# Kernel optimization log

Measured on AMD Instinct MI355X. Metric: run time of the kernel, lower is better.

Reference implementation:

```python
import jax, jax.numpy as jnp
import numpy as np

B, T, C, H, NC = 512, 256, 512, 512, 96  # batch, encoder steps, channels, hidden, num classes


def setup_inputs() -> dict:
    key = jax.random.key(0)
    ks = jax.random.split(key, 12)
    def w(k, shape, fan):
        return (jax.random.normal(k, shape, jnp.float32) / np.sqrt(fan)).astype(jnp.float32)
    labels = jax.random.randint(ks[0], (B,), 0, NC)
    return {
        "prev_h": jax.random.normal(ks[1], (B, H), jnp.float32),
        "prev_c": jax.random.normal(ks[2], (B, H), jnp.float32),
        "batch_H": jax.random.normal(ks[3], (B, T, C), jnp.float32),
        "char_onehots": jax.nn.one_hot(labels, NC, dtype=jnp.float32),
        "Wi": w(ks[4], (C, H), C),            # i2h kernel (no bias)
        "Wh": w(ks[5], (H, H), H),            # h2h kernel
        "bh": jnp.zeros((H,), jnp.float32),    # h2h bias
        "Ws": w(ks[6], (H, 1), H),            # score kernel (no bias)
        "K": w(ks[7], (C + NC, 4 * H), C + NC),  # LSTM input kernel (i,f,g,o)
        "R": w(ks[8], (H, 4 * H), H),            # LSTM recurrent kernel
        "b": jnp.zeros((4 * H,), jnp.float32),    # LSTM bias
    }


def reference(prev_h, prev_c, batch_H, char_onehots, Wi, Wh, bh, Ws, K, R, b):
    # Additive (Bahdanau) attention
    proj = jnp.einsum('btc,ch->bth', batch_H, Wi)                  # [B,T,H]
    hp = prev_h @ Wh + bh                                          # [B,H]
    e = jnp.einsum('bth,h->bt', jnp.tanh(proj + hp[:, None, :]), Ws[:, 0])  # [B,T]
    alpha = jax.nn.softmax(e, axis=1)                              # [B,T]
    context = jnp.einsum('bt,btc->bc', alpha, batch_H)             # [B,C]
    # LSTMCell step (keras gate order: i, f, g, o; sigmoid recurrent act, tanh act)
    x = jnp.concatenate([context, char_onehots], axis=1)           # [B,C+NC]
    z = x @ K + prev_h @ R + b                                     # [B,4H]
    i, f, g, o = jnp.split(z, 4, axis=1)
    c_new = jax.nn.sigmoid(f) * prev_c + jax.nn.sigmoid(i) * jnp.tanh(g)
    h_new = jax.nn.sigmoid(o) * jnp.tanh(c_new)
    return (h_new, c_new, alpha[:, :, None])  # ((h,c), alpha[B,T,1])
```

## Files before the change

kernel.cpp:

```cpp
#include <hip/hip_runtime.h>
#include <hip/hip_bf16.h>
#include <stdint.h>

#define KFULL 1120
#define N4H   2048
#define MTOT  131072

typedef float f32x4 __attribute__((ext_vector_type(4)));
typedef __bf16 bf16x8 __attribute__((ext_vector_type(8)));
typedef unsigned short u16;

__device__ __forceinline__ u16 f2bf_bits(float f){
  __bf16 b = (__bf16)f;
  union { __bf16 b; u16 u; } cv; cv.b = b;
  return cv.u;
}
__device__ __forceinline__ float sigf(float x){ return 1.f / (1.f + __expf(-x)); }
__device__ __forceinline__ float tanh_fast(float x){ return 1.f - 2.f / (__expf(2.f * x) + 1.f); }
__device__ __forceinline__ int swz(int row){ return (row ^ (row >> 2)) & 3; }

__global__ void prep_w(const float* __restrict__ Wi, const float* __restrict__ Wh,
                       const float* __restrict__ Km, const float* __restrict__ R,
                       u16* __restrict__ wiT, u16* __restrict__ whT, u16* __restrict__ wfT){
  int idx = blockIdx.x * 256 + threadIdx.x;
  if (idx < 524288){
    const float* src = (idx < 262144) ? Wi : Wh;
    u16* dst = (idx < 262144) ? wiT : whT;
    int e = idx & 262143;
    int n = e & 511, kk = (e >> 9) & 31, s = e >> 14;
    float v = src[(size_t)(s * 32 + kk) * 512 + n];
    int dkk = (idx < 262144) ? kk
            : ((kk & 7) | ((((kk >> 3) ^ swz(n)) & 3) << 3));
    dst[((size_t)s * 512 + n) * 32 + dkk] = f2bf_bits(v);
  } else {
    int e = idx - 524288;
    if (e >= 35 * 2048 * 32) return;
    int n = e & 2047, kk = (e >> 11) & 31, s = e >> 16;
    int k = s * 32 + kk;
    float v = (k < 608) ? Km[(size_t)k * 2048 + n] : R[(size_t)(k - 608) * 2048 + n];
    int dkk = (kk & 7) | ((((kk >> 3) ^ swz(n)) & 3) << 3);
    wfT[((size_t)s * 2048 + n) * 32 + dkk] = f2bf_bits(v);
  }
}

__global__ void prep_x(const float* __restrict__ onehots, const float* __restrict__ prev_h,
                       float* __restrict__ x_full){
  int idx = blockIdx.x * 256 + threadIdx.x;
  if (idx >= 512 * 608) return;
  int b = idx / 608, c = idx % 608;
  float v = (c < 96) ? onehots[b * 96 + c] : prev_h[b * 512 + (c - 96)];
  x_full[(size_t)b * KFULL + 512 + c] = v;
}

__launch_bounds__(256, 3)
__global__ void gemm_small(const float* __restrict__ A, int lda, int ksteps,
                           const u16* __restrict__ Bt, int ntot,
                           float* __restrict__ outp, size_t partStride){
  __shared__ u16 smA[128 * 32];
  __shared__ u16 smB[128 * 32];

  const int tid  = threadIdx.x;
  const int lane = tid & 63, w = tid >> 6;
  const int wr = w >> 1, wc = w & 1;
  const int fr = lane & 15, g = lane >> 4;
  const int m0 = blockIdx.x * 128;
  const int n0 = blockIdx.y * 128;
  const int s0 = blockIdx.z * ksteps;
  outp += (size_t)blockIdx.z * partStride;

  f32x4 acc[4][4] = {};

  const int ar = tid >> 2;
  const int ac = (tid & 3) * 8;
  const float* ap = A + (size_t)(m0 + ar) * lda + ac;
  const int sz  = swz(ar);
  const int ab0 = ar * 64 + (((tid & 3) ^ sz) << 4);
  const int ab1 = ab0 + 64 * 64;

  for (int s = 0; s < ksteps; ++s){
    const int kc = (s0 + s) * 32;
    const char* bsrc = (const char*)Bt + ((size_t)(s0 + s) * ntot + n0) * 64;
    #pragma unroll
    for (int j = 0; j < 2; ++j){
      int off = w * 2048 + j * 1024;
      __builtin_amdgcn_global_load_lds(
        (const __attribute__((address_space(1))) void*)(bsrc + off + lane * 16),
        (__attribute__((address_space(3))) void*)((char*)smB + off),
        16, 0, 0);
    }
    float4 a0 = *(const float4*)(ap + kc);
    float4 a1 = *(const float4*)(ap + kc + 4);
    float4 a2 = *(const float4*)(ap + (size_t)64 * lda + kc);
    float4 a3 = *(const float4*)(ap + (size_t)64 * lda + kc + 4);
    bf16x8 w0, w1;
    w0[0]=(__bf16)a0.x; w0[1]=(__bf16)a0.y; w0[2]=(__bf16)a0.z; w0[3]=(__bf16)a0.w;
    w0[4]=(__bf16)a1.x; w0[5]=(__bf16)a1.y; w0[6]=(__bf16)a1.z; w0[7]=(__bf16)a1.w;
    w1[0]=(__bf16)a2.x; w1[1]=(__bf16)a2.y; w1[2]=(__bf16)a2.z; w1[3]=(__bf16)a2.w;
    w1[4]=(__bf16)a3.x; w1[5]=(__bf16)a3.y; w1[6]=(__bf16)a3.z; w1[7]=(__bf16)a3.w;
    *(bf16x8*)((char*)smA + ab0) = w0;
    *(bf16x8*)((char*)smA + ab1) = w1;
    __syncthreads();

    bf16x8 af[4];
    #pragma unroll
    for (int m = 0; m < 4; ++m){
      int rl = wr * 64 + m * 16 + fr;
      af[m] = *(const bf16x8*)((const char*)smA + rl * 64 + ((g ^ swz(rl)) << 4));
    }
    #pragma unroll
    for (int n = 0; n < 4; ++n){
      int nl = wc * 64 + n * 16 + fr;
      bf16x8 bfv = *(const bf16x8*)((const char*)smB + nl * 64 + ((g ^ swz(nl)) << 4));
      #pragma unroll
      for (int m = 0; m < 4; ++m)
        acc[m][n] = __builtin_amdgcn_mfma_f32_16x16x32_bf16(af[m], bfv, acc[m][n], 0, 0, 0);
    }
    __syncthreads();
  }

  #pragma unroll
  for (int n = 0; n < 4; ++n){
    int col = n0 + wc * 64 + n * 16 + fr;
    #pragma unroll
    for (int m = 0; m < 4; ++m){
      int row = m0 + wr * 64 + m * 16 + g * 4;
      #pragma unroll
      for (int j = 0; j < 4; ++j)
        outp[(size_t)(row + j) * ntot + col] = acc[m][n][j];
    }
  }
}

__launch_bounds__(256, 2)
__global__ void gemm_attn(const float* __restrict__ A,
                          const u16* __restrict__ Bt,
                          const float* __restrict__ hpart,
                          const float* __restrict__ bh,
                          const float* __restrict__ Wsv,
                          float* __restrict__ epart){
  __shared__ u16 smA[16][64 * 32];

  const int tid  = threadIdx.x;
  const int lane = tid & 63, w = tid >> 6;
  const int fr = lane & 15, g = lane >> 4;
  const int bid = blockIdx.x;
  const int m0 = (bid >> 1) * 64;
  const int nb = bid & 1;
  const int n0 = nb * 256;
  const int b  = m0 >> 8;

  const int arow = tid >> 2;
  const float* ag = A + (size_t)(m0 + arow) * 512 + (tid & 3) * 8;
  const int awbase = arow * 64 + (((tid & 3) ^ swz(arow)) << 4);
  float4 av[32];
  #pragma unroll
  for (int s = 0; s < 16; ++s){
    av[2 * s]     = *(const float4*)(ag + s * 32);
    av[2 * s + 1] = *(const float4*)(ag + s * 32 + 4);
  }
  #pragma unroll
  for (int s = 0; s < 16; ++s){
    bf16x8 v;
    v[0]=(__bf16)av[2*s].x;   v[1]=(__bf16)av[2*s].y;
    v[2]=(__bf16)av[2*s].z;   v[3]=(__bf16)av[2*s].w;
    v[4]=(__bf16)av[2*s+1].x; v[5]=(__bf16)av[2*s+1].y;
    v[6]=(__bf16)av[2*s+1].z; v[7]=(__bf16)av[2*s+1].w;
    *(bf16x8*)((char*)&smA[s][0] + awbase) = v;
  }

  float hpv[4], wsv[4];
  #pragma unroll
  for (int n = 0; n < 4; ++n){
    int col = n0 + w * 64 + n * 16 + fr;
    float h = bh[col];
    #pragma unroll
    for (int p = 0; p < 4; ++p) h += hpart[(size_t)p * 262144 + (size_t)b * 512 + col];
    hpv[n] = h;
    wsv[n] = Wsv[col];
  }

  __syncthreads();

  const u16* bbase = Bt + ((size_t)(n0 + w * 64 + fr)) * 32 + g * 8;
  bf16x8 bA[4], bB[4];
  #pragma unroll
  for (int nf = 0; nf < 4; ++nf)
    bA[nf] = *(const bf16x8*)(bbase + (size_t)nf * 16 * 32);

  f32x4 acc[4][4] = {};

  #pragma unroll
  for (int s = 0; s < 16; ++s){
    if (s + 1 < 16){
      if ((s & 1) == 0){
        #pragma unroll
        for (int nf = 0; nf < 4; ++nf)
          bB[nf] = *(const bf16x8*)(bbase + ((size_t)(s + 1) * 512 + nf * 16) * 32);
      } else {
        #pragma unroll
        for (int nf = 0; nf < 4; ++nf)
          bA[nf] = *(const bf16x8*)(bbase + ((size_t)(s + 1) * 512 + nf * 16) * 32);
      }
    }
    bf16x8 af[4];
    #pragma unroll
    for (int m = 0; m < 4; ++m){
      int rl = m * 16 + fr;
      af[m] = *(const bf16x8*)((const char*)&smA[s][0] + rl * 64 + ((g ^ swz(rl)) << 4));
    }
    #pragma unroll
    for (int n = 0; n < 4; ++n){
      bf16x8 bfv = ((s & 1) == 0) ? bA[n] : bB[n];
      #pragma unroll
      for (int m = 0; m < 4; ++m)
        acc[m][n] = __builtin_amdgcn_mfma_f32_16x16x32_bf16(af[m], bfv, acc[m][n], 0, 0, 0);
    }
  }

  float p[16] = {};
  #pragma unroll
  for (int n = 0; n < 4; ++n){
    #pragma unroll
    for (int m = 0; m < 4; ++m)
      #pragma unroll
      for (int j = 0; j < 4; ++j)
        p[m * 4 + j] += tanh_fast(acc[m][n][j] + hpv[n]) * wsv[n];
  }
  #pragma unroll
  for (int mask = 1; mask < 16; mask <<= 1)
    #pragma unroll
    for (int i = 0; i < 16; ++i)
      p[i] += __shfl_xor(p[i], mask);

  float* smRed = (float*)&smA[0][0];
  __syncthreads();
  if (fr == 0){
    #pragma unroll
    for (int m = 0; m < 4; ++m)
      #pragma unroll
      for (int j = 0; j < 4; ++j)
        smRed[w * 64 + m * 16 + g * 4 + j] = p[m * 4 + j];
  }
  __syncthreads();
  if (tid < 64)
    epart[(size_t)nb * MTOT + m0 + tid] =
      smRed[tid] + smRed[64 + tid] + smRed[128 + tid] + smRed[192 + tid];
}

__global__ void ctx_softmax(const float* __restrict__ epart, const float* __restrict__ batch_H,
                            float* __restrict__ x_full, float* __restrict__ alpha_out){
  __shared__ float sa[256];
  __shared__ float red[4], red2[4];
  __shared__ f32x4 sred[8][32];
  int b = blockIdx.x, q = blockIdx.y, tid = threadIdx.x;

  float e = epart[(size_t)b * 256 + tid] + epart[MTOT + (size_t)b * 256 + tid];
  float m = e;
  #pragma unroll
  for (int mask = 1; mask < 64; mask <<= 1) m = fmaxf(m, __shfl_xor(m, mask));
  int w = tid >> 6;
  if ((tid & 63) == 0) red[w] = m;
  __syncthreads();
  m = fmaxf(fmaxf(red[0], red[1]), fmaxf(red[2], red[3]));
  float ev = __expf(e - m);
  float s = ev;
  #pragma unroll
  for (int mask = 1; mask < 64; mask <<= 1) s += __shfl_xor(s, mask);
  if ((tid & 63) == 0) red2[w] = s;
  __syncthreads();
  s = red2[0] + red2[1] + red2[2] + red2[3];
  float a = ev / s;
  sa[tid] = a;
  if (q == 0) alpha_out[(size_t)b * 256 + tid] = a;
  __syncthreads();

  int c4 = tid & 31, tq = tid >> 5;
  const float4* bhp = (const float4*)(batch_H + (size_t)b * 131072) + (size_t)tq * 32 * 128 + q * 32 + c4;
  f32x4 acc = {0.f, 0.f, 0.f, 0.f};
  #pragma unroll 4
  for (int t = 0; t < 32; ++t){
    float av = sa[tq * 32 + t];
    float4 v = bhp[(size_t)t * 128];
    acc[0] += av * v.x; acc[1] += av * v.y; acc[2] += av * v.z; acc[3] += av * v.w;
  }
  sred[tq][c4] = acc;
  __syncthreads();
  if (tid < 32){
    f32x4 o = sred[0][tid];
    #pragma unroll
    for (int r = 1; r < 8; ++r){
      f32x4 v = sred[r][tid];
      o[0] += v[0]; o[1] += v[1]; o[2] += v[2]; o[3] += v[3];
    }
    float4 st; st.x = o[0]; st.y = o[1]; st.z = o[2]; st.w = o[3];
    *(float4*)(x_full + (size_t)b * KFULL + q * 128 + tid * 4) = st;
  }
}

__global__ void gates_k(const float* __restrict__ zpart, const float* __restrict__ bias,
                        const float* __restrict__ prev_c, float* __restrict__ out){
  int idx = blockIdx.x * 256 + threadIdx.x;
  int b = idx >> 9, h = idx & 511;
  float zi = bias[h], zf = bias[512 + h], zg = bias[1024 + h], zo = bias[1536 + h];
  #pragma unroll
  for (int p = 0; p < 5; ++p){
    const float* zr = zpart + (size_t)p * 1048576 + (size_t)b * N4H;
    zi += zr[h]; zf += zr[512 + h]; zg += zr[1024 + h]; zo += zr[1536 + h];
  }
  float c = sigf(zf) * prev_c[idx] + sigf(zi) * tanh_fast(zg);
  float hn = sigf(zo) * tanh_fast(c);
  out[idx] = hn;
  out[262144 + idx] = c;
}

extern "C" void kernel_launch(void* const* d_in, const int* in_sizes, int n_in,
                              void* d_out, int out_size, void* d_ws, size_t ws_size,
                              hipStream_t stream){
  const float* prev_h  = (const float*)d_in[0];
  const float* prev_c  = (const float*)d_in[1];
  const float* batch_H = (const float*)d_in[2];
  const float* onehots = (const float*)d_in[3];
  const float* Wi      = (const float*)d_in[4];
  const float* Wh      = (const float*)d_in[5];
  const float* bh      = (const float*)d_in[6];
  const float* Ws      = (const float*)d_in[7];
  const float* Km      = (const float*)d_in[8];
  const float* R       = (const float*)d_in[9];
  const float* bb      = (const float*)d_in[10];
  float* out = (float*)d_out;

  char* ws = (char*)d_ws;
  u16*  wiT    = (u16*)(ws + 0);
  u16*  whT    = (u16*)(ws + 524288);
  u16*  wfT    = (u16*)(ws + 1048576);
  float* hpart = (float*)(ws + 5636096);
  float* epart = (float*)(ws + 9830400);
  float* x_full= (float*)(ws + 11927552);
  float* zpart = (float*)(ws + 14221312);

  float* alpha = out + 524288;

  prep_w<<<11008, 256, 0, stream>>>(Wi, Wh, Km, R, wiT, whT, wfT);
  prep_x<<<1216, 256, 0, stream>>>(onehots, prev_h, x_full);
  gemm_small<<<dim3(4, 4, 4), 256, 0, stream>>>(prev_h, 512, 4, whT, 512,
                                                hpart, 262144);
  gemm_attn<<<4096, 256, 0, stream>>>(batch_H, wiT, hpart, bh, Ws, epart);
  ctx_softmax<<<dim3(512, 4), 256, 0, stream>>>(epart, batch_H, x_full, alpha);
  gemm_small<<<dim3(4, 16, 5), 256, 0, stream>>>(x_full, KFULL, 7, wfT, N4H,
                                                 zpart, 1048576);
  gates_k<<<1024, 256, 0, stream>>>(zpart, bb, prev_c, out);
}
```

Baseline: 245.4 us.

## Restructure attention GEMM with double-buffered LDS pipeline and larger tiles

The attention projection GEMM now uses 512-thread blocks with 128x256 tiles. B tiles are streamed into double-buffered LDS with global_load_lds, and A tiles are prefetched through registers in a software pipeline over K chunks of 64. The Wi weights are pre-laid out in a swizzled 64-wide K tiled format, and block IDs are remapped for locality. The aim is to hide global-load latency and raise reuse of A and B per block. The cost is more LDS per block and reliance on manual waitcnt ordering.

```diff
diff --git a/kernel.cpp b/kernel.cpp
--- a/kernel.cpp
+++ b/kernel.cpp
@@ -21,17 +21,20 @@
 
 __global__ void prep_w(const float* __restrict__ Wi, const float* __restrict__ Wh,
                        const float* __restrict__ Km, const float* __restrict__ R,
-                       u16* __restrict__ wiT, u16* __restrict__ whT, u16* __restrict__ wfT){
+                       u16* __restrict__ wiT2, u16* __restrict__ whT, u16* __restrict__ wfT){
   int idx = blockIdx.x * 256 + threadIdx.x;
-  if (idx < 524288){
-    const float* src = (idx < 262144) ? Wi : Wh;
-    u16* dst = (idx < 262144) ? wiT : whT;
-    int e = idx & 262143;
+  if (idx < 262144){
+    int col = idx & 511, kk = (idx >> 9) & 63, t = idx >> 15;
+    float v = Wi[(size_t)(t * 64 + kk) * 512 + col];
+    size_t dst = ((size_t)(t * 2 + (col >> 8)) * 256 + (col & 255)) * 64
+               + (size_t)(((kk >> 3) ^ (col & 7)) * 8 + (kk & 7));
+    wiT2[dst] = f2bf_bits(v);
+  } else if (idx < 524288){
+    int e = idx - 262144;
     int n = e & 511, kk = (e >> 9) & 31, s = e >> 14;
-    float v = src[(size_t)(s * 32 + kk) * 512 + n];
-    int dkk = (idx < 262144) ? kk
-            : ((kk & 7) | ((((kk >> 3) ^ swz(n)) & 3) << 3));
-    dst[((size_t)s * 512 + n) * 32 + dkk] = f2bf_bits(v);
+    float v = Wh[(size_t)(s * 32 + kk) * 512 + n];
+    int dkk = (kk & 7) | ((((kk >> 3) ^ swz(n)) & 3) << 3);
+    whT[((size_t)s * 512 + n) * 32 + dkk] = f2bf_bits(v);
   } else {
     int e = idx - 524288;
     if (e >= 35 * 2048 * 32) return;
@@ -131,47 +134,31 @@
   }
 }
 
-__launch_bounds__(256, 2)
+__launch_bounds__(512, 2)
 __global__ void gemm_attn(const float* __restrict__ A,
-                          const u16* __restrict__ Bt,
+                          const u16* __restrict__ Bt2,
                           const float* __restrict__ hpart,
                           const float* __restrict__ bh,
                           const float* __restrict__ Wsv,
                           float* __restrict__ epart){
-  __shared__ u16 smA[16][64 * 32];
+  __shared__ u16 bufA[2][128 * 64];
+  __shared__ u16 bufB[2][256 * 64];
+  __shared__ float smRed[4][128];
 
   const int tid  = threadIdx.x;
   const int lane = tid & 63, w = tid >> 6;
+  const int wr = w >> 2, wc = w & 3;
   const int fr = lane & 15, g = lane >> 4;
-  const int bid = blockIdx.x;
-  const int m0 = (bid >> 1) * 64;
-  const int nb = bid & 1;
-  const int n0 = nb * 256;
+
+  const int sid = (blockIdx.x & 7) * 256 + (blockIdx.x >> 3);
+  const int mb = sid >> 1, nb = sid & 1;
+  const int m0 = mb * 128, n0 = nb * 256;
   const int b  = m0 >> 8;
 
-  const int arow = tid >> 2;
-  const float* ag = A + (size_t)(m0 + arow) * 512 + (tid & 3) * 8;
-  const int awbase = arow * 64 + (((tid & 3) ^ swz(arow)) << 4);
-  float4 av[32];
-  #pragma unroll
-  for (int s = 0; s < 16; ++s){
-    av[2 * s]     = *(const float4*)(ag + s * 32);
-    av[2 * s + 1] = *(const float4*)(ag + s * 32 + 4);
-  }
-  #pragma unroll
-  for (int s = 0; s < 16; ++s){
-    bf16x8 v;
-    v[0]=(__bf16)av[2*s].x;   v[1]=(__bf16)av[2*s].y;
-    v[2]=(__bf16)av[2*s].z;   v[3]=(__bf16)av[2*s].w;
-    v[4]=(__bf16)av[2*s+1].x; v[5]=(__bf16)av[2*s+1].y;
-    v[6]=(__bf16)av[2*s+1].z; v[7]=(__bf16)av[2*s+1].w;
-    *(bf16x8*)((char*)&smA[s][0] + awbase) = v;
-  }
-
   float hpv[4], wsv[4];
   #pragma unroll
   for (int n = 0; n < 4; ++n){
-    int col = n0 + w * 64 + n * 16 + fr;
+    int col = n0 + wc * 64 + n * 16 + fr;
     float h = bh[col];
     #pragma unroll
     for (int p = 0; p < 4; ++p) h += hpart[(size_t)p * 262144 + (size_t)b * 512 + col];
@@ -179,43 +166,92 @@
     wsv[n] = Wsv[col];
   }
 
-  __syncthreads();
-
-  const u16* bbase = Bt + ((size_t)(n0 + w * 64 + fr)) * 32 + g * 8;
-  bf16x8 bA[4], bB[4];
-  #pragma unroll
-  for (int nf = 0; nf < 4; ++nf)
-    bA[nf] = *(const bf16x8*)(bbase + (size_t)nf * 16 * 32);
+  const int arow = tid >> 2, q = tid & 3;
+  const float* ag = A + (size_t)(m0 + arow) * 512 + q * 16;
+  const int aw0 = arow * 128 + (((2 * q)     ^ (arow & 7)) << 4);
+  const int aw1 = arow * 128 + (((2 * q + 1) ^ (arow & 7)) << 4);
+
+  const int fs = fr & 7;
 
   f32x4 acc[4][4] = {};
-
-  #pragma unroll
-  for (int s = 0; s < 16; ++s){
-    if (s + 1 < 16){
-      if ((s & 1) == 0){
-        #pragma unroll
-        for (int nf = 0; nf < 4; ++nf)
-          bB[nf] = *(const bf16x8*)(bbase + ((size_t)(s + 1) * 512 + nf * 16) * 32);
-      } else {
-        #pragma unroll
-        for (int nf = 0; nf < 4; ++nf)
-          bA[nf] = *(const bf16x8*)(bbase + ((size_t)(s + 1) * 512 + nf * 16) * 32);
-      }
-    }
-    bf16x8 af[4];
-    #pragma unroll
-    for (int m = 0; m < 4; ++m){
-      int rl = m * 16 + fr;
-      af[m] = *(const bf16x8*)((const char*)&smA[s][0] + rl * 64 + ((g ^ swz(rl)) << 4));
-    }
-    #pragma unroll
-    for (int n = 0; n < 4; ++n){
-      bf16x8 bfv = ((s & 1) == 0) ? bA[n] : bB[n];
-      #pragma unroll
-      for (int m = 0; m < 4; ++m)
-        acc[m][n] = __builtin_amdgcn_mfma_f32_16x16x32_bf16(af[m], bfv, acc[m][n], 0, 0, 0);
-    }
-  }
+  float4 paE[4], paO[4];
+
+#define ISSUE_B(t, c) do {                                                  \
+    const char* bsrc = (const char*)Bt2 + ((size_t)((t) * 2 + nb)) * 32768; \
+    _Pragma("unroll")                                                       \
+    for (int j = 0; j < 4; ++j){                                            \
+      int off = w * 4096 + j * 1024;                                        \
+      __builtin_amdgcn_global_load_lds(                                     \
+        (const __attribute__((address_space(1))) void*)(bsrc + off + lane * 16), \
+        (__attribute__((address_space(3))) void*)((char*)&bufB[c][0] + off),\
+        16, 0, 0);                                                          \
+    }                                                                       \
+  } while(0)
+
+#define ISSUE_A(t, R) do {                                                  \
+    const float* s_ = ag + (size_t)(t) * 64;                                \
+    R[0] = *(const float4*)(s_);                                            \
+    R[1] = *(const float4*)(s_ + 4);                                        \
+    R[2] = *(const float4*)(s_ + 8);                                        \
+    R[3] = *(const float4*)(s_ + 12);                                       \
+  } while(0)
+
+#define WRITE_A(R, c) do {                                                  \
+    bf16x8 v0, v1;                                                          \
+    v0[0]=(__bf16)R[0].x; v0[1]=(__bf16)R[0].y; v0[2]=(__bf16)R[0].z; v0[3]=(__bf16)R[0].w; \
+    v0[4]=(__bf16)R[1].x; v0[5]=(__bf16)R[1].y; v0[6]=(__bf16)R[1].z; v0[7]=(__bf16)R[1].w; \
+    v1[0]=(__bf16)R[2].x; v1[1]=(__bf16)R[2].y; v1[2]=(__bf16)R[2].z; v1[3]=(__bf16)R[2].w; \
+    v1[4]=(__bf16)R[3].x; v1[5]=(__bf16)R[3].y; v1[6]=(__bf16)R[3].z; v1[7]=(__bf16)R[3].w; \
+    *(bf16x8*)((char*)&bufA[c][0] + aw0) = v0;                              \
+    *(bf16x8*)((char*)&bufA[c][0] + aw1) = v1;                              \
+  } while(0)
+
+#define HALF(c, h2) do {                                                    \
+    bf16x8 af[4], bf[4];                                                    \
+    _Pragma("unroll")                                                       \
+    for (int m = 0; m < 4; ++m){                                            \
+      int row = wr * 64 + m * 16 + fr;                                      \
+      af[m] = *(const bf16x8*)((const char*)&bufA[c][0] + row * 128 + ((((h2) * 4 + g) ^ fs) << 4)); \
+    }                                                                       \
+    _Pragma("unroll")                                                       \
+    for (int n = 0; n < 4; ++n){                                            \
+      int col = wc * 64 + n * 16 + fr;                                      \
+      bf[n] = *(const bf16x8*)((const char*)&bufB[c][0] + col * 128 + ((((h2) * 4 + g) ^ fs) << 4)); \
+    }                                                                       \
+    __builtin_amdgcn_s_setprio(1);                                          \
+    _Pragma("unroll")                                                       \
+    for (int n = 0; n < 4; ++n)                                             \
+      _Pragma("unroll")                                                     \
+      for (int m = 0; m < 4; ++m)                                           \
+        acc[m][n] = __builtin_amdgcn_mfma_f32_16x16x32_bf16(af[m], bf[n], acc[m][n], 0, 0, 0); \
+    __builtin_amdgcn_s_setprio(0);                                          \
+  } while(0)
+
+  __syncthreads();
+  ISSUE_B(0, 0);
+  ISSUE_A(0, paE);
+  WRITE_A(paE, 0);
+  ISSUE_A(1, paO);
+
+  #pragma unroll
+  for (int t = 0; t < 8; ++t){
+    const int c = t & 1;
+    if (t < 7) asm volatile("s_waitcnt vmcnt(4)" ::: "memory");
+    else       asm volatile("s_waitcnt vmcnt(0)" ::: "memory");
+    asm volatile("s_waitcnt lgkmcnt(0)" ::: "memory");
+    __builtin_amdgcn_s_barrier();
+    asm volatile("" ::: "memory");
+    if (t + 1 < 8) ISSUE_B(t + 1, c ^ 1);
+    if (t + 2 < 8) { if (t & 1) ISSUE_A(t + 2, paO); else ISSUE_A(t + 2, paE); }
+    HALF(c, 0);
+    if (t + 1 < 8) { if (t & 1) WRITE_A(paE, c ^ 1); else WRITE_A(paO, c ^ 1); }
+    HALF(c, 1);
+  }
+
+#undef ISSUE_B
+#undef ISSUE_A
+#undef WRITE_A
+#undef HALF
 
   float p[16] = {};
   #pragma unroll
@@ -231,20 +267,18 @@
     #pragma unroll
     for (int i = 0; i < 16; ++i)
       p[i] += __shfl_xor(p[i], mask);
-
-  float* smRed = (float*)&smA[0][0];
   __syncthreads();
   if (fr == 0){
     #pragma unroll
     for (int m = 0; m < 4; ++m)
       #pragma unroll
       for (int j = 0; j < 4; ++j)
-        smRed[w * 64 + m * 16 + g * 4 + j] = p[m * 4 + j];
-  }
-  __syncthreads();
-  if (tid < 64)
+        smRed[wc][wr * 64 + m * 16 + g * 4 + j] = p[m * 4 + j];
+  }
+  __syncthreads();
+  if (tid < 128)
     epart[(size_t)nb * MTOT + m0 + tid] =
-      smRed[tid] + smRed[64 + tid] + smRed[128 + tid] + smRed[192 + tid];
+      smRed[0][tid] + smRed[1][tid] + smRed[2][tid] + smRed[3][tid];
 }
 
 __global__ void ctx_softmax(const float* __restrict__ epart, const float* __restrict__ batch_H,
@@ -330,7 +364,7 @@
   float* out = (float*)d_out;
 
   char* ws = (char*)d_ws;
-  u16*  wiT    = (u16*)(ws + 0);
+  u16*  wiT2   = (u16*)(ws + 0);
   u16*  whT    = (u16*)(ws + 524288);
   u16*  wfT    = (u16*)(ws + 1048576);
   float* hpart = (float*)(ws + 5636096);
@@ -340,11 +374,11 @@
 
   float* alpha = out + 524288;
 
-  prep_w<<<11008, 256, 0, stream>>>(Wi, Wh, Km, R, wiT, whT, wfT);
+  prep_w<<<11008, 256, 0, stream>>>(Wi, Wh, Km, R, wiT2, whT, wfT);
   prep_x<<<1216, 256, 0, stream>>>(onehots, prev_h, x_full);
   gemm_small<<<dim3(4, 4, 4), 256, 0, stream>>>(prev_h, 512, 4, whT, 512,
                                                 hpart, 262144);
-  gemm_attn<<<4096, 256, 0, stream>>>(batch_H, wiT, hpart, bh, Ws, epart);
+  gemm_attn<<<2048, 512, 0, stream>>>(batch_H, wiT2, hpart, bh, Ws, epart);
   ctx_softmax<<<dim3(512, 4), 256, 0, stream>>>(epart, batch_H, x_full, alpha);
   gemm_small<<<dim3(4, 16, 5), 256, 0, stream>>>(x_full, KFULL, 7, wfT, N4H,
                                                  zpart, 1048576);
```

Result: no change. 243.5 us (-0.8%).
